# Performance work log

Measured on AMD Instinct MI355X. Metric: run time of the kernel, lower is better.

The kernel has to match this reference:

```python
import jax, jax.numpy as jnp
import numpy as np
import math

EMBED_DIM = 1024
BATCH = 4
SEQ = 2048


def setup_inputs() -> dict:
    key = jax.random.key(0)
    ks = jax.random.split(key, 7)
    d = EMBED_DIM
    s = 1.0 / math.sqrt(d)
    x = jax.random.normal(ks[0], (BATCH, SEQ, d), dtype=jnp.float32)
    Wq = jax.random.normal(ks[1], (d, d), dtype=jnp.float32) * s
    Wk = jax.random.normal(ks[2], (d, d), dtype=jnp.float32) * s
    Wv = jax.random.normal(ks[3], (d, d), dtype=jnp.float32) * s
    bq = jax.random.normal(ks[4], (d,), dtype=jnp.float32) * 0.01
    bk = jax.random.normal(ks[5], (d,), dtype=jnp.float32) * 0.01
    bv = jax.random.normal(ks[6], (d,), dtype=jnp.float32) * 0.01
    return {"x": x, "Wq": Wq, "bq": bq, "Wk": Wk, "bk": bk, "Wv": Wv, "bv": bv}


def reference(x, Wq, bq, Wk, bk, Wv, bv):
    # q/k/v: [B, S, D] linear projections (weights stored as [in, out])
    q = jnp.einsum('bsd,de->bse', x, Wq) + bq
    k = jnp.einsum('bsd,de->bse', x, Wk) + bk
    v = jnp.einsum('bsd,de->bse', x, Wv) + bv
    scale = jnp.sqrt(jnp.asarray(x.shape[-1], dtype=x.dtype))
    # full O(S^2) score matrix, as in the original (non-fused) attention
    attn_scores = jnp.einsum('bqd,bkd->bqk', q, k) / scale
    attn_probs = jax.nn.softmax(attn_scores, axis=-1)
    # lxa.strassen(attn_probs, v) is a (Strassen) matmul: same math as matmul
    return jnp.einsum('bqk,bkd->bqd', attn_probs, v)
```

## Files before the change

### kernel.cpp

```cpp
#include <hip/hip_runtime.h>
#include <stdint.h>

#define SEQ 2048
#define DIM 1024
#define NB 4
#define MTOT (NB*SEQ)
#define QKVN (3*DIM)

typedef __attribute__((ext_vector_type(8))) short short8;
typedef __attribute__((ext_vector_type(4))) float f32x4;

__device__ __forceinline__ unsigned short f2b(float f) {
    union { float f; unsigned int u; } v; v.f = f;
    return (unsigned short)((v.u + 0x7FFFu + ((v.u >> 16) & 1u)) >> 16);
}
__device__ __forceinline__ float b2f(unsigned short u) {
    union { unsigned int i; float f; } v; v.i = ((unsigned int)u) << 16; return v.f;
}

__device__ __forceinline__ void gload_lds16(const unsigned short* g, unsigned short* l) {
    __builtin_amdgcn_global_load_lds(
        (const __attribute__((address_space(1))) void*)g,
        (__attribute__((address_space(3))) void*)l, 16, 0, 0);
}

__device__ __forceinline__ short8 ds128(unsigned addr) {
    short8 r;
    asm volatile("ds_read_b128 %0, %1" : "=v"(r) : "v"(addr));
    return r;
}

#define FENCE_BARRIER do { asm volatile("" ::: "memory"); \
    __builtin_amdgcn_s_barrier(); asm volatile("" ::: "memory"); } while (0)
#define SB __builtin_amdgcn_sched_barrier(0)

__device__ __forceinline__ int xcd_swz(int bid, int nwg) {
    if (nwg & 7) return bid;
    return (bid & 7) * (nwg >> 3) + (bid >> 3);
}


__global__ __launch_bounds__(256)
void cast_kernel(const float* __restrict__ in, unsigned short* __restrict__ out, int nchunk) {
    int i = blockIdx.x * 256 + threadIdx.x;
    if (i >= nchunk) return;
    float4 a = ((const float4*)in)[i*2];
    float4 b = ((const float4*)in)[i*2+1];
    union { unsigned short u[8]; uint4 v; } r;
    r.u[0]=f2b(a.x); r.u[1]=f2b(a.y); r.u[2]=f2b(a.z); r.u[3]=f2b(a.w);
    r.u[4]=f2b(b.x); r.u[5]=f2b(b.y); r.u[6]=f2b(b.z); r.u[7]=f2b(b.w);
    ((uint4*)out)[i] = r.v;
}

__global__ __launch_bounds__(256)
void transpose_cast3(const float* __restrict__ w0, const float* __restrict__ w1,
                     const float* __restrict__ w2, unsigned short* __restrict__ out) {
    const float* in = (blockIdx.y == 0) ? w0 : (blockIdx.y == 1) ? w1 : w2;
    unsigned short* o = out + (size_t)blockIdx.y * DIM * DIM;
    __shared__ unsigned short tile[64][66];
    int tpc = DIM >> 6;
    int tr = ((int)blockIdx.x / tpc) << 6;
    int tc = ((int)blockIdx.x % tpc) << 6;
    int t = threadIdx.x;
    #pragma unroll
    for (int i = 0; i < 16; i++) {
        int idx = t + i*256;
        int r = idx >> 6, c = idx & 63;
        tile[r][c] = f2b(in[(size_t)(tr + r)*DIM + tc + c]);
    }
    __syncthreads();
    #pragma unroll
    for (int i = 0; i < 16; i++) {
        int idx = t + i*256;
        int r = idx >> 6, c = idx & 63;
        o[(size_t)(tc + r)*DIM + tr + c] = tile[c][r];
    }
}

__global__ __launch_bounds__(256)
void bias_concat(const float* __restrict__ bq, const float* __restrict__ bk,
                 const float* __restrict__ bv, float* __restrict__ o) {
    int i = blockIdx.x*256 + threadIdx.x;
    float v = (i < DIM) ? bq[i] : ((i < 2*DIM) ? bk[i-DIM] : bv[i-2*DIM]);
    o[i] = v;
}


__device__ __forceinline__ void stageA64(const unsigned short* __restrict__ Xb, int ldx,
                                         unsigned short* dstBase, int k0,
                                         int tid, int wid) {
    int srow = tid >> 3;
    int scol = ((tid & 7) ^ (srow & 7)) << 3;
    gload_lds16(Xb + (size_t)srow*ldx + k0 + scol, dstBase + wid*512);
}

__device__ __forceinline__ void stageB(const unsigned short* __restrict__ Xb, int ldx,
                                       unsigned short* dstBase, int h, int k0,
                                       int tid, int wid) {
    int srow = tid >> 3;
    int scol = ((tid & 7) ^ (srow & 7)) << 3;
    const unsigned short* g = Xb + (size_t)(h*128 + srow)*ldx + k0 + scol;
    unsigned short* d = dstBase + h*8192 + wid*512;
    gload_lds16(g, d);
    gload_lds16(g + (size_t)64*ldx, d + 4096);
}

#define RD_A(BUF) do { _Pragma("unroll") for (int mf = 0; mf < 2; ++mf) { \
    fa[mf][0] = ds128(As0 + (BUF)*8192u + aRow + mf*2048u + c0); \
    fa[mf][1] = ds128(As0 + (BUF)*8192u + aRow + mf*2048u + c1); } } while (0)

#define RD_B(BUF, QN) do { _Pragma("unroll") for (int nf = 0; nf < 2; ++nf) { \
    fb[nf][0] = ds128(Bs0 + (BUF)*32768u + (QN)*16384u + bRow + nf*2048u + c0); \
    fb[nf][1] = ds128(Bs0 + (BUF)*32768u + (QN)*16384u + bRow + nf*2048u + c1); } } while (0)

#define MMA_PH(QN) do { \
    asm volatile("s_waitcnt lgkmcnt(0)" ::: "memory"); \
    __builtin_amdgcn_sched_barrier(0); \
    __builtin_amdgcn_s_setprio(1); \
    _Pragma("unroll") for (int mf = 0; mf < 2; ++mf) \
      _Pragma("unroll") for (int nf = 0; nf < 2; ++nf) \
        _Pragma("unroll") for (int ks = 0; ks < 2; ++ks) \
          acc[QN][mf][nf] = __builtin_amdgcn_mfma_f32_16x16x32_bf16( \
              fa[mf][ks], fb[nf][ks], acc[QN][mf][nf], 0, 0, 0); \
    __builtin_amdgcn_s_setprio(0); \
} while (0)

template<int MODE>
__global__ __launch_bounds__(512, 2)
void gemm4p(const unsigned short* __restrict__ A, int lda, size_t sA,
            const unsigned short* __restrict__ Bt, int ldb, size_t sB,
            float* __restrict__ aux,
            void* __restrict__ Cout, int ldc, size_t sC,
            int N, int K, float scale,
            unsigned short* __restrict__ vtout, int nT)
{
    __shared__ __align__(16) unsigned short As[2][4096];
    __shared__ __align__(16) unsigned short Bs[2][16384];
    int nbn = N >> 8;
    int bid = xcd_swz((int)blockIdx.x, (int)gridDim.x);
    int bm = bid / nbn, bn = bid % nbn;
    int bz = blockIdx.y;
    int tid = threadIdx.x;
    int lane = tid & 63;
    int wid  = tid >> 6;
    int wm = (wid >> 2) & 1;
    int wn = wid & 3;
    int rlo = lane & 15;
    int shi = lane >> 4;

    unsigned As0 = (unsigned)(uintptr_t)&As[0][0];
    unsigned Bs0 = (unsigned)(uintptr_t)&Bs[0][0];
    unsigned c0 = (unsigned)(((shi     ^ rlo) & 7) * 16);
    unsigned c1 = (unsigned)((((4+shi) ^ rlo) & 7) * 16);
    unsigned aRow = (unsigned)((wm*32 + rlo) * 128);
    unsigned bRow = (unsigned)((wn*32 + rlo) * 128);

    f32x4 acc[2][2][2];
    #pragma unroll
    for (int a = 0; a < 2; a++)
        #pragma unroll
        for (int b = 0; b < 2; b++)
            #pragma unroll
            for (int c = 0; c < 2; c++)
                acc[a][b][c] = (f32x4){0.f,0.f,0.f,0.f};

    const unsigned short* Ab = A + sA*bz + (size_t)(bm*64)*lda;
    const unsigned short* Bb = Bt + sB*bz + (size_t)(bn*256)*ldb;

    stageA64(Ab, lda, &As[0][0], 0, tid, wid);
    stageB(Bb, ldb, &Bs[0][0], 0, 0,  tid, wid);
    stageB(Bb, ldb, &Bs[0][0], 1, 0,  tid, wid);
    stageA64(Ab, lda, &As[1][0], 64, tid, wid);
    stageB(Bb, ldb, &Bs[1][0], 0, 64, tid, wid);
    SB;
    asm volatile("s_waitcnt vmcnt(3)" ::: "memory");
    FENCE_BARRIER;

    short8 fa[2][2], fb[2][2];
    int nt = K >> 6;
    int nit = nt >> 1;

    for (int it = 0; it < nit; ++it) {
        int kO  = (2*it + 1) << 6;
        int kE2 = (2*it + 2 < nt) ? (2*it + 2) << 6 : 0;
        int kO2 = (2*it + 3 < nt) ? (2*it + 3) << 6 : 0;

        RD_A(0); RD_B(0, 0);
        stageB(Bb, ldb, &Bs[1][0], 1, kO, tid, wid);
        asm volatile("s_waitcnt lgkmcnt(4)" ::: "memory");
        FENCE_BARRIER; MMA_PH(0); FENCE_BARRIER;
        RD_B(0, 1);
        stageA64(Ab, lda, &As[0][0], kE2, tid, wid);
        stageB(Bb, ldb, &Bs[0][0], 0, kE2, tid, wid);
        SB;
        asm volatile("s_waitcnt vmcnt(3)" ::: "memory");
        FENCE_BARRIER; MMA_PH(1); FENCE_BARRIER;
        RD_A(1); RD_B(1, 0);
        stageB(Bb, ldb, &Bs[0][0], 1, kE2, tid, wid);
        asm volatile("s_waitcnt lgkmcnt(4)" ::: "memory");
        FENCE_BARRIER; MMA_PH(0); FENCE_BARRIER;
        RD_B(1, 1);
        stageA64(Ab, lda, &As[1][0], kO2, tid, wid);
        stageB(Bb, ldb, &Bs[1][0], 0, kO2, tid, wid);
        SB;
        asm volatile("s_waitcnt vmcnt(3)" ::: "memory");
        FENCE_BARRIER; MMA_PH(1); FENCE_BARRIER;
    }

    asm volatile("s_waitcnt vmcnt(0)" ::: "memory");
    FENCE_BARRIER;

    int r0 = shi << 2;
    unsigned short* Cu = (unsigned short*)Cout + sC*bz;
    float* Cf = (float*)Cout + sC*bz;

    if constexpr (MODE == 2) {
        float rs[2][4];
        #pragma unroll
        for (int mf = 0; mf < 2; ++mf)
            #pragma unroll
            for (int r = 0; r < 4; ++r) rs[mf][r] = 0.f;
        #pragma unroll
        for (int qn = 0; qn < 2; ++qn)
            #pragma unroll
            for (int mf = 0; mf < 2; ++mf)
                #pragma unroll
                for (int nf = 0; nf < 2; ++nf) {
                    int col = bn*256 + qn*128 + wn*32 + nf*16 + rlo;
                    #pragma unroll
                    for (int r = 0; r < 4; ++r) {
                        int row = bm*64 + wm*32 + mf*16 + r0 + r;
                        float u = __expf(acc[qn][mf][nf][r] * scale);
                        Cu[(size_t)row*ldc + col] = f2b(u);
                        rs[mf][r] += u;
                    }
                }
        #pragma unroll
        for (int m = 1; m < 16; m <<= 1)
            #pragma unroll
            for (int mf = 0; mf < 2; ++mf)
                #pragma unroll
                for (int r = 0; r < 4; ++r)
                    rs[mf][r] += __shfl_xor(rs[mf][r], m);
        float* redL = (float*)&As[0][0];
        if (rlo == 0) {
            #pragma unroll
            for (int mf = 0; mf < 2; ++mf)
                #pragma unroll
                for (int r = 0; r < 4; ++r)
                    redL[(wm*32 + mf*16 + (shi<<2) + r)*5 + wn] = rs[mf][r];
        }
        __syncthreads();
        if (tid < 64) {
            float s = redL[tid*5+0] + redL[tid*5+1] + redL[tid*5+2] + redL[tid*5+3];
            aux[((size_t)bz*SEQ + bm*64 + tid)*8 + bn] = s;
        }
        return;
    }

    if constexpr (MODE == 3) {
        float inv[2][4];
        #pragma unroll
        for (int mf = 0; mf < 2; ++mf)
            #pragma unroll
            for (int r = 0; r < 4; ++r) {
                int row = bm*64 + wm*32 + mf*16 + r0 + r;
                const float* pp = aux + ((size_t)bz*SEQ + row)*8;
                float s = pp[0]+pp[1]+pp[2]+pp[3]+pp[4]+pp[5]+pp[6]+pp[7];
                inv[mf][r] = 1.0f / s;
            }
        #pragma unroll
        for (int qn = 0; qn < 2; ++qn)
            #pragma unroll
            for (int mf = 0; mf < 2; ++mf)
                #pragma unroll
                for (int nf = 0; nf < 2; ++nf) {
                    int col = bn*256 + qn*128 + wn*32 + nf*16 + rlo;
                    #pragma unroll
                    for (int r = 0; r < 4; ++r) {
                        int row = bm*64 + wm*32 + mf*16 + r0 + r;
                        Cf[(size_t)row*ldc + col] = acc[qn][mf][nf][r] * inv[mf][r];
                    }
                }
        return;
    }

    if (bn < nT) {
        #pragma unroll
        for (int qn = 0; qn < 2; ++qn)
            #pragma unroll
            for (int mf = 0; mf < 2; ++mf)
                #pragma unroll
                for (int nf = 0; nf < 2; ++nf) {
                    int col = bn*256 + qn*128 + wn*32 + nf*16 + rlo;
                    float badd = aux[col];
                    #pragma unroll
                    for (int r = 0; r < 4; ++r) {
                        int row = bm*64 + wm*32 + mf*16 + r0 + r;
                        Cu[(size_t)row*ldc + col] = f2b(acc[qn][mf][nf][r] + badd);
                    }
                }
    } else {
        #pragma unroll
        for (int qn = 0; qn < 2; ++qn)
            #pragma unroll
            for (int mf = 0; mf < 2; ++mf)
                #pragma unroll
                for (int nf = 0; nf < 2; ++nf) {
                    int col  = bn*256 + qn*128 + wn*32 + nf*16 + rlo;
                    int colv = col - nT*256;
                    float badd = aux[col];
                    int row = bm*64 + wm*32 + mf*16 + r0;
                    int b  = row >> 11, sr = row & 2047;
                    ushort4 w;
                    w.x = f2b(acc[qn][mf][nf][0] + badd);
                    w.y = f2b(acc[qn][mf][nf][1] + badd);
                    w.z = f2b(acc[qn][mf][nf][2] + badd);
                    w.w = f2b(acc[qn][mf][nf][3] + badd);
                    *(ushort4*)(vtout + (size_t)b*DIM*SEQ + (size_t)colv*SEQ + sr) = w;
                }
    }
}

extern "C" void kernel_launch(void* const* d_in, const int* in_sizes, int n_in,
                              void* d_out, int out_size, void* d_ws, size_t ws_size,
                              hipStream_t stream)
{
    (void)in_sizes; (void)n_in; (void)out_size;
    const float* x  = (const float*)d_in[0];
    const float* Wq = (const float*)d_in[1];
    const float* bq = (const float*)d_in[2];
    const float* Wk = (const float*)d_in[3];
    const float* bk = (const float*)d_in[4];
    const float* Wv = (const float*)d_in[5];
    const float* bv = (const float*)d_in[6];
    float* out = (float*)d_out;

    unsigned short* qkv = (unsigned short*)d_ws;
    unsigned short* vt  = qkv + (size_t)MTOT*QKVN;
    float* biasc = (float*)(vt + (size_t)NB*DIM*SEQ);
    char* ovl = (char*)biasc + 65536;
    unsigned short* xb    = (unsigned short*)ovl;
    unsigned short* wqkvt = xb + (size_t)MTOT*DIM;
    unsigned short* scoresB = (unsigned short*)ovl;

    size_t base = (size_t)MTOT*QKVN*2 + (size_t)NB*DIM*SEQ*2 + 65536;
    int bpp = 1;
    if (base + 4*((size_t)SEQ*SEQ*2 + SEQ*32) <= ws_size) bpp = 4;
    else if (base + 2*((size_t)SEQ*SEQ*2 + SEQ*32) <= ws_size) bpp = 2;
    float* psum = (float*)(scoresB + (size_t)bpp*SEQ*SEQ);

    cast_kernel<<<MTOT*DIM/8/256, 256, 0, stream>>>(x, xb, MTOT*DIM/8);
    transpose_cast3<<<dim3(256, 3), 256, 0, stream>>>(Wq, Wk, Wv, wqkvt);
    bias_concat<<<QKVN/256, 256, 0, stream>>>(bq, bk, bv, biasc);

    gemm4p<0><<<dim3((MTOT/64)*(QKVN/256)), 512, 0, stream>>>(
        xb, DIM, 0, wqkvt, DIM, 0, biasc, qkv, QKVN, 0, QKVN, DIM, 1.f, vt, 8);

    const float scl = 1.0f / 32.0f;
    for (int p = 0; p < NB; p += bpp) {
        const unsigned short* qp = qkv + (size_t)p*SEQ*QKVN;
        gemm4p<2><<<dim3((SEQ/64)*(SEQ/256), bpp), 512, 0, stream>>>(
            qp,       QKVN, (size_t)SEQ*QKVN,
            qp + DIM, QKVN, (size_t)SEQ*QKVN,
            psum, scoresB, SEQ, (size_t)SEQ*SEQ, SEQ, DIM, scl, nullptr, 0);
        gemm4p<3><<<dim3((SEQ/64)*(DIM/256), bpp), 512, 0, stream>>>(
            scoresB, SEQ, (size_t)SEQ*SEQ,
            vt + (size_t)p*DIM*SEQ, SEQ, (size_t)DIM*SEQ,
            psum, out + (size_t)p*SEQ*DIM, DIM, (size_t)SEQ*DIM, DIM, SEQ, 1.f, nullptr, 0);
    }
}
```

Measured before the change: 169.0 us.

## Merge prep kernels into one launch and stage V-transpose stores through LDS

The three preprocessing kernels (x cast, weight transpose-cast, bias concat) are merged into a single launch that dispatches on block index, removing two kernel launches and their gaps. In the QKV GEMM epilogue, the V tile is now written transposed into a swizzled LDS buffer and then stored to global memory with 16-byte coalesced rows, instead of scattered 8-byte strided writes. This reuses the B shared-memory buffer after the main loop and adds a barrier.

```diff
diff --git a/kernel.cpp b/kernel.cpp
--- a/kernel.cpp
+++ b/kernel.cpp
@@ -39,50 +39,55 @@
     return (bid & 7) * (nwg >> 3) + (bid >> 3);
 }
 
-
 __global__ __launch_bounds__(256)
-void cast_kernel(const float* __restrict__ in, unsigned short* __restrict__ out, int nchunk) {
-    int i = blockIdx.x * 256 + threadIdx.x;
-    if (i >= nchunk) return;
-    float4 a = ((const float4*)in)[i*2];
-    float4 b = ((const float4*)in)[i*2+1];
-    union { unsigned short u[8]; uint4 v; } r;
-    r.u[0]=f2b(a.x); r.u[1]=f2b(a.y); r.u[2]=f2b(a.z); r.u[3]=f2b(a.w);
-    r.u[4]=f2b(b.x); r.u[5]=f2b(b.y); r.u[6]=f2b(b.z); r.u[7]=f2b(b.w);
-    ((uint4*)out)[i] = r.v;
-}
-
-__global__ __launch_bounds__(256)
-void transpose_cast3(const float* __restrict__ w0, const float* __restrict__ w1,
-                     const float* __restrict__ w2, unsigned short* __restrict__ out) {
-    const float* in = (blockIdx.y == 0) ? w0 : (blockIdx.y == 1) ? w1 : w2;
-    unsigned short* o = out + (size_t)blockIdx.y * DIM * DIM;
+void prep(const float* __restrict__ x,
+          const float* __restrict__ Wq, const float* __restrict__ Wk,
+          const float* __restrict__ Wv,
+          const float* __restrict__ bq, const float* __restrict__ bk,
+          const float* __restrict__ bv,
+          unsigned short* __restrict__ xb, unsigned short* __restrict__ wqkvt,
+          float* __restrict__ biasc)
+{
     __shared__ unsigned short tile[64][66];
-    int tpc = DIM >> 6;
-    int tr = ((int)blockIdx.x / tpc) << 6;
-    int tc = ((int)blockIdx.x % tpc) << 6;
+    int b = blockIdx.x;
     int t = threadIdx.x;
-    #pragma unroll
-    for (int i = 0; i < 16; i++) {
-        int idx = t + i*256;
-        int r = idx >> 6, c = idx & 63;
-        tile[r][c] = f2b(in[(size_t)(tr + r)*DIM + tc + c]);
-    }
-    __syncthreads();
-    #pragma unroll
-    for (int i = 0; i < 16; i++) {
-        int idx = t + i*256;
-        int r = idx >> 6, c = idx & 63;
-        o[(size_t)(tc + r)*DIM + tr + c] = tile[c][r];
-    }
-}
-
-__global__ __launch_bounds__(256)
-void bias_concat(const float* __restrict__ bq, const float* __restrict__ bk,
-                 const float* __restrict__ bv, float* __restrict__ o) {
-    int i = blockIdx.x*256 + threadIdx.x;
+    if (b < 4096) {
+        int i = b*256 + t;
+        float4 a = ((const float4*)x)[(size_t)i*2];
+        float4 c = ((const float4*)x)[(size_t)i*2+1];
+        union { unsigned short u[8]; uint4 v; } r;
+        r.u[0]=f2b(a.x); r.u[1]=f2b(a.y); r.u[2]=f2b(a.z); r.u[3]=f2b(a.w);
+        r.u[4]=f2b(c.x); r.u[5]=f2b(c.y); r.u[6]=f2b(c.z); r.u[7]=f2b(c.w);
+        ((uint4*)xb)[i] = r.v;
+        return;
+    }
+    if (b < 4864) {
+        int bb = b - 4096;
+        int y = bb >> 8;
+        int bx = bb & 255;
+        const float* in = (y == 0) ? Wq : (y == 1) ? Wk : Wv;
+        unsigned short* o = wqkvt + (size_t)y * DIM * DIM;
+        int tpc = DIM >> 6;
+        int tr = (bx / tpc) << 6;
+        int tc = (bx % tpc) << 6;
+        #pragma unroll
+        for (int i = 0; i < 16; i++) {
+            int idx = t + i*256;
+            int r = idx >> 6, c = idx & 63;
+            tile[r][c] = f2b(in[(size_t)(tr + r)*DIM + tc + c]);
+        }
+        __syncthreads();
+        #pragma unroll
+        for (int i = 0; i < 16; i++) {
+            int idx = t + i*256;
+            int r = idx >> 6, c = idx & 63;
+            o[(size_t)(tc + r)*DIM + tr + c] = tile[c][r];
+        }
+        return;
+    }
+    int i = (b - 4864)*256 + t;
     float v = (i < DIM) ? bq[i] : ((i < 2*DIM) ? bk[i-DIM] : bv[i-2*DIM]);
-    o[i] = v;
+    biasc[i] = v;
 }
 
 
@@ -301,6 +306,7 @@
                     }
                 }
     } else {
+        unsigned short* vtile = &Bs[0][0];
         #pragma unroll
         for (int qn = 0; qn < 2; ++qn)
             #pragma unroll
@@ -308,17 +314,29 @@
                 #pragma unroll
                 for (int nf = 0; nf < 2; ++nf) {
                     int col  = bn*256 + qn*128 + wn*32 + nf*16 + rlo;
-                    int colv = col - nT*256;
+                    int colv = qn*128 + wn*32 + nf*16 + rlo;
                     float badd = aux[col];
-                    int row = bm*64 + wm*32 + mf*16 + r0;
-                    int b  = row >> 11, sr = row & 2047;
+                    int sl0 = wm*32 + mf*16 + r0;
                     ushort4 w;
                     w.x = f2b(acc[qn][mf][nf][0] + badd);
                     w.y = f2b(acc[qn][mf][nf][1] + badd);
                     w.z = f2b(acc[qn][mf][nf][2] + badd);
                     w.w = f2b(acc[qn][mf][nf][3] + badd);
-                    *(ushort4*)(vtout + (size_t)b*DIM*SEQ + (size_t)colv*SEQ + sr) = w;
+                    unsigned off = (unsigned)colv*128u + (((unsigned)sl0*2u) ^ (((unsigned)colv & 7u) << 4));
+                    *(ushort4*)((char*)vtile + off) = w;
                 }
+        __syncthreads();
+        int b  = (bm*64) >> 11;
+        int sr = (bm*64) & 2047;
+        unsigned short* vtb = vtout + (size_t)b*DIM*SEQ + (size_t)((bn - nT)*256)*SEQ + sr;
+        #pragma unroll
+        for (int i = 0; i < 4; ++i) {
+            int cl = i*64 + (tid >> 3);
+            int so = (tid & 7) * 8;
+            unsigned off = (unsigned)cl*128u + (((unsigned)so*2u) ^ (((unsigned)cl & 7u) << 4));
+            short8 vv = *(short8*)((char*)vtile + off);
+            *(short8*)(vtb + (size_t)cl*SEQ + so) = vv;
+        }
     }
 }
 
@@ -350,9 +368,7 @@
     else if (base + 2*((size_t)SEQ*SEQ*2 + SEQ*32) <= ws_size) bpp = 2;
     float* psum = (float*)(scoresB + (size_t)bpp*SEQ*SEQ);
 
-    cast_kernel<<<MTOT*DIM/8/256, 256, 0, stream>>>(x, xb, MTOT*DIM/8);
-    transpose_cast3<<<dim3(256, 3), 256, 0, stream>>>(Wq, Wk, Wv, wqkvt);
-    bias_concat<<<QKVN/256, 256, 0, stream>>>(bq, bk, bv, biasc);
+    prep<<<4876, 256, 0, stream>>>(x, Wq, Wk, Wv, bq, bk, bv, xb, wqkvt, biasc);
 
     gemm4p<0><<<dim3((MTOT/64)*(QKVN/256)), 512, 0, stream>>>(
         xb, DIM, 0, wqkvt, DIM, 0, biasc, qkv, QKVN, 0, QKVN, DIM, 1.f, vt, 8);
```

After: 165.4 us. 2.2% less time.
